# Kernel optimization log

Measured on AMD Instinct MI355X. Metric: run time of the kernel, lower is better.

Reference implementation:

```python
import jax, jax.numpy as jnp
import numpy as np

B, S, D = 4, 4096, 1024
DK, DV = 64, 64

def setup_inputs() -> dict:
    key = jax.random.key(0)
    ks = jax.random.split(key, 4)
    scale = 1.0 / np.sqrt(D)
    x = jax.random.normal(ks[0], (B, S, D), dtype=jnp.float32)
    Wq = jax.random.normal(ks[1], (DK, D), dtype=jnp.float32) * scale
    Wk = jax.random.normal(ks[2], (DK, D), dtype=jnp.float32) * scale
    Wv = jax.random.normal(ks[3], (DV, D), dtype=jnp.float32) * scale
    bq = jnp.zeros((DK,), jnp.float32)
    bk = jnp.zeros((DK,), jnp.float32)
    bv = jnp.zeros((DV,), jnp.float32)
    return {"x": x, "Wq": Wq, "bq": bq, "Wk": Wk, "bk": bk, "Wv": Wv, "bv": bv}

def reference(x, Wq, bq, Wk, bk, Wv, bv):
    # Linear projections (torch nn.Linear: y = x @ W.T + b)
    Q = jnp.einsum('bsd,kd->bsk', x, Wq) + bq      # [B,S,DK]
    K = jnp.einsum('bsd,kd->bsk', x, Wk) + bk      # [B,S,DK]
    V = jnp.einsum('bsd,vd->bsv', x, Wv) + bv      # [B,S,DV]
    scale = 1.0 / jnp.sqrt(jnp.float32(DK))
    scores = jnp.einsum('bqk,bsk->bqs', Q, K) * scale  # [B,S,S]
    attn = jax.nn.softmax(scores, axis=-1)
    return jnp.einsum('bqs,bsv->bqv', attn, V)     # [B,S,DV]
```

## Files before the change

### kernel.cpp

```cpp
#include <hip/hip_runtime.h>

typedef unsigned int uint;
typedef unsigned short ushort;

#define SQ 4096
#define DMODEL 1024
#define DH 64
#define NQ 16384
#define L2E 1.4426950408889634f
#define QSCALE (0.125f * 1.4426950408889634f)

typedef __attribute__((ext_vector_type(4))) float f32x4;
typedef __attribute__((ext_vector_type(8))) short bf16x8;

#if __has_builtin(__builtin_amdgcn_exp2f)
#define EXP2(x) __builtin_amdgcn_exp2f(x)
#else
#define EXP2(x) exp2f(x)
#endif


__device__ __forceinline__ void ld_lds16(const ushort* g, ushort* l) {
    __builtin_amdgcn_global_load_lds(
        (const __attribute__((address_space(1))) void*)g,
        (__attribute__((address_space(3))) void*)l, 16, 0, 0);
}

__device__ __forceinline__ void split2(float x, ushort& h, ushort& l) {
    uint u = __float_as_uint(x);
    float lof = x - __uint_as_float(u & 0xffff0000u);
    h = (ushort)(u >> 16);
    l = (ushort)(__float_as_uint(lof) >> 16);
}

__device__ __forceinline__ ushort bf16rne(float a) {
    uint ua = __float_as_uint(a);
    return (ushort)((ua + 0x7fffu + ((ua >> 16) & 1u)) >> 16);
}

__device__ __forceinline__ uint bfpack_rne(float a, float b) {
    uint ua = __float_as_uint(a);
    ua = (ua + 0x7fffu + ((ua >> 16) & 1u)) >> 16;
    uint ub = __float_as_uint(b);
    ub = (ub + 0x7fffu + ((ub >> 16) & 1u)) & 0xffff0000u;
    return ua | ub;
}

__global__ __launch_bounds__(256) void wsplit_kernel(
    const float* __restrict__ Wq, const float* __restrict__ Wk,
    const float* __restrict__ Wv, ushort* __restrict__ Wch)
{
    int r = blockIdx.x;
    int k = threadIdx.x * 4;
    const float* src = (r < 64)  ? (Wq + r * DMODEL)
                     : (r < 128) ? (Wk + (r - 64) * DMODEL)
                     :             (Wv + (r - 128) * DMODEL);
    float4 v = *(const float4*)&src[k];
    ushort h[4] = {bf16rne(v.x), bf16rne(v.y), bf16rne(v.z), bf16rne(v.w)};
    int ch = k >> 6, kl = k & 63;
    int g = kl >> 3;
    int idx = ch * 12288 + r * 64 + ((g ^ (r & 7)) << 3) + (kl & 7);
    *(ushort4*)&Wch[idx] = make_ushort4(h[0], h[1], h[2], h[3]);
}

__global__ __launch_bounds__(256, 1) void proj_kernel(
    const float* __restrict__ x, const ushort* __restrict__ Wch,
    const float* __restrict__ bq, const float* __restrict__ bk,
    const float* __restrict__ bv,
    ushort* __restrict__ Qr, ushort* __restrict__ Kr,
    ushort* __restrict__ Vh, ushort* __restrict__ Vl)
{
    extern __shared__ ushort sm[];

    const int tid  = threadIdx.x;
    const int w    = tid >> 6;
    const int l    = tid & 63;
    const int ln   = l & 15;
    const int quad = l >> 4;
    const int r0   = blockIdx.x << 6;
    const int xr   = tid >> 4;
    const int xc4  = tid & 15;

    f32x4 o_[4][3];
    #pragma unroll
    for (int mt = 0; mt < 4; ++mt)
        #pragma unroll
        for (int nt = 0; nt < 3; ++nt) o_[mt][nt] = (f32x4)0.f;

    float4 xv[4];
    #pragma unroll
    for (int i = 0; i < 4; ++i)
        xv[i] = *(const float4*)&x[(r0 + i * 16 + xr) * DMODEL + xc4 * 4];
    {
        const ushort* gh = Wch + w * 3072 + l * 8;
        ushort* dh = sm + 16384 + w * 3072;
        #pragma unroll
        for (int i = 0; i < 6; ++i) ld_lds16(gh + i * 512, dh + i * 512);
    }
    #pragma unroll
    for (int i = 0; i < 4; ++i) {
        int r = i * 16 + xr;
        ushort h0, h1, h2, h3, l0, l1, l2, l3;
        split2(xv[i].x, h0, l0); split2(xv[i].y, h1, l1);
        split2(xv[i].z, h2, l2); split2(xv[i].w, h3, l3);
        int idx = r * 64 + (((xc4 >> 1) ^ (r & 7)) << 3) + (xc4 & 1) * 4;
        *(ushort4*)&sm[idx]        = make_ushort4(h0, h1, h2, h3);
        *(ushort4*)&sm[4096 + idx] = make_ushort4(l0, l1, l2, l3);
    }

    for (int ch = 0; ch < 16; ++ch) {
        const int cur = ch & 1, nxt = cur ^ 1;
        __syncthreads();
        if (ch + 1 < 16) {
            const ushort* gh = Wch + (ch + 1) * 12288 + w * 3072 + l * 8;
            ushort* dh = sm + 16384 + nxt * 12288 + w * 3072;
            #pragma unroll
            for (int i = 0; i < 6; ++i) ld_lds16(gh + i * 512, dh + i * 512);
            #pragma unroll
            for (int i = 0; i < 4; ++i)
                xv[i] = *(const float4*)&x[(r0 + i * 16 + xr) * DMODEL +
                                           (ch + 1) * 64 + xc4 * 4];
        }
        const ushort* Xh = sm + cur * 8192;
        const ushort* Xl = Xh + 4096;
        const ushort* Wh = sm + 16384 + cur * 12288;
        #pragma unroll
        for (int kc = 0; kc < 2; ++kc) {
            int gsw = ((kc * 4 + quad) ^ (ln & 7)) << 3;
            bf16x8 xh[4], xl[4], wh[3];
            #pragma unroll
            for (int mt = 0; mt < 4; ++mt) {
                int off = (mt * 16 + ln) * 64 + gsw;
                xh[mt] = *(bf16x8*)&Xh[off];
                xl[mt] = *(bf16x8*)&Xl[off];
            }
            #pragma unroll
            for (int nt = 0; nt < 3; ++nt)
                wh[nt] = *(bf16x8*)&Wh[(w * 48 + nt * 16 + ln) * 64 + gsw];
            #pragma unroll
            for (int mt = 0; mt < 4; ++mt)
                #pragma unroll
                for (int nt = 0; nt < 3; ++nt) {
                    o_[mt][nt] = __builtin_amdgcn_mfma_f32_16x16x32_bf16(
                        xh[mt], wh[nt], o_[mt][nt], 0, 0, 0);
                    o_[mt][nt] = __builtin_amdgcn_mfma_f32_16x16x32_bf16(
                        xl[mt], wh[nt], o_[mt][nt], 0, 0, 0);
                }
        }
        if (ch + 1 < 16) {
            #pragma unroll
            for (int i = 0; i < 4; ++i) {
                int r = i * 16 + xr;
                ushort h0, h1, h2, h3, l0, l1, l2, l3;
                split2(xv[i].x, h0, l0); split2(xv[i].y, h1, l1);
                split2(xv[i].z, h2, l2); split2(xv[i].w, h3, l3);
                int idx = nxt * 8192 + r * 64 +
                          (((xc4 >> 1) ^ (r & 7)) << 3) + (xc4 & 1) * 4;
                *(ushort4*)&sm[idx]        = make_ushort4(h0, h1, h2, h3);
                *(ushort4*)&sm[4096 + idx] = make_ushort4(l0, l1, l2, l3);
            }
        }
    }

    __syncthreads();
    uint* Oqk = (uint*)sm;
    uint* Ov  = (uint*)sm + 8192;
    #pragma unroll
    for (int nt = 0; nt < 3; ++nt) {
        int col = 16 * (3 * w + nt) + ln;
        float bias, scl;
        if (col < 64)       { bias = bq[col];       scl = QSCALE; }
        else if (col < 128) { bias = bk[col - 64];  scl = 1.f; }
        else                { bias = bv[col - 128]; scl = 1.f; }
        #pragma unroll
        for (int mt = 0; mt < 4; ++mt)
            #pragma unroll
            for (int j = 0; j < 4; ++j) {
                int m = mt * 16 + quad * 4 + j;
                float val = (o_[mt][nt][j] + bias) * scl;
                if (col < 128) {
                    Oqk[m * 128 + col] = (uint)bf16rne(val);
                } else {
                    int v = col - 128;
                    uint u = __float_as_uint(val);
                    float lof = val - __uint_as_float(u & 0xffff0000u);
                    Ov[v * 64 + (m ^ ((v & 7) << 2))] =
                        (__float_as_uint(lof) & 0xffff0000u) | (u >> 16);
                }
            }
    }
    __syncthreads();
    const int tile_qk = r0 >> 6;
    #pragma unroll
    for (int i = 0; i < 8; ++i) {
        int id = i * 256 + tid;
        int m = id >> 5, g = id & 31;
        uint4 e = *(uint4*)&Oqk[m * 128 + g * 4];
        uint h0 = (e.x & 0xffffu) | (e.y << 16);
        uint h1 = (e.z & 0xffffu) | (e.w << 16);
        int gg = g & 15;
        int idx = tile_qk * 4096 + m * 64 +
                  (((gg >> 1) ^ (m & 7)) << 3) + (gg & 1) * 4;
        uint2 hh; hh.x = h0; hh.y = h1;
        if (g < 16) *(uint2*)&Qr[idx] = hh;
        else        *(uint2*)&Kr[idx] = hh;
    }
    const int b  = r0 >> 12;
    const int vt = b * 64 + ((r0 & (SQ - 1)) >> 6);
    #pragma unroll
    for (int i = 0; i < 4; ++i) {
        int id = i * 256 + tid;
        int v = id >> 4, gm = id & 15;
        uint4 e = *(uint4*)&Ov[v * 64 + 4 * (gm ^ (v & 7))];
        uint h0 = (e.x & 0xffffu) | (e.y << 16);
        uint h1 = (e.z & 0xffffu) | (e.w << 16);
        uint l0 = (e.x >> 16) | (e.y & 0xffff0000u);
        uint l1 = (e.z >> 16) | (e.w & 0xffff0000u);
        int idx = vt * 4096 + v * 64 + (((gm >> 1) ^ (v & 7)) << 3) + (gm & 1) * 4;
        uint2 hh; hh.x = h0; hh.y = h1;
        uint2 llv; llv.x = l0; llv.y = l1;
        *(uint2*)&Vh[idx] = hh; *(uint2*)&Vl[idx] = llv;
    }
}

__global__ __launch_bounds__(256, 2) void attn_kernel(
    const ushort* __restrict__ Qr, const ushort* __restrict__ Kr,
    const ushort* __restrict__ Vh, const ushort* __restrict__ Vl,
    float* __restrict__ opart, float* __restrict__ lpart,
    float* __restrict__ out, int ks)
{
    __shared__ ushort As[32768];

    const int tid  = threadIdx.x;
    const int w    = tid >> 6;
    const int l    = tid & 63;
    const int ln   = l & 15;
    const int quad = l >> 4;

    const int bid   = blockIdx.x;
    const int qb    = bid / ks;
    const int c     = bid - qb * ks;
    const int q0    = qb << 7;
    const int b     = q0 >> 12;
    const int chunk = SQ / ks;
    const int tile0 = (b * SQ + c * chunk) >> 6;
    const int vt0   = b * 64 + ((c * chunk) >> 6);
    const int nIter = chunk >> 6;

    {
        const ushort* gq = Qr + (q0 >> 6) * 4096 + w * 2048 + l * 8;
        #pragma unroll
        for (int i = 0; i < 4; ++i)
            ld_lds16(gq + i * 512, As + w * 2048 + i * 512);
    }
    __syncthreads();
    bf16x8 qf[2][2];
    #pragma unroll
    for (int nt = 0; nt < 2; ++nt)
        #pragma unroll
        for (int kc = 0; kc < 2; ++kc) {
            int row = w * 32 + nt * 16 + ln;
            qf[nt][kc] = *(bf16x8*)&As[row * 64 +
                                       (((kc * 4 + quad) ^ (ln & 7)) << 3)];
        }
    __syncthreads();

    {
        int kt = tile0 * 4096 + w * 1024 + l * 8;
        int vt = vt0 * 4096 + w * 1024 + l * 8;
        ld_lds16(Kr + kt,       As + w * 1024);
        ld_lds16(Kr + kt + 512, As + w * 1024 + 512);
        ld_lds16(Vh + vt,       As + 4096 + w * 1024);
        ld_lds16(Vh + vt + 512, As + 4096 + w * 1024 + 512);
        ld_lds16(Vl + vt,       As + 8192 + w * 1024);
        ld_lds16(Vl + vt + 512, As + 8192 + w * 1024 + 512);
    }

    float l_[2] = {0.f, 0.f};
    f32x4 o_[4][2];
    #pragma unroll
    for (int mt = 0; mt < 4; ++mt)
        #pragma unroll
        for (int nt = 0; nt < 2; ++nt) o_[mt][nt] = (f32x4)0.f;

    for (int it = 0; it < nIter; ++it) {
        const int cur = it & 1, nxt = cur ^ 1;
        __syncthreads();
        if (it + 1 < nIter) {
            int kt = (tile0 + it + 1) * 4096 + w * 1024 + l * 8;
            int vt = (vt0 + it + 1) * 4096 + w * 1024 + l * 8;
            ushort* bb = As + nxt * 12288;
            ld_lds16(Kr + kt,       bb + w * 1024);
            ld_lds16(Kr + kt + 512, bb + w * 1024 + 512);
            ld_lds16(Vh + vt,       bb + 4096 + w * 1024);
            ld_lds16(Vh + vt + 512, bb + 4096 + w * 1024 + 512);
            ld_lds16(Vl + vt,       bb + 8192 + w * 1024);
            ld_lds16(Vl + vt + 512, bb + 8192 + w * 1024 + 512);
        }
        const ushort* Ks  = As + cur * 12288;
        const ushort* Vhs = Ks + 4096;
        const ushort* Vls = Ks + 8192;
        ushort* Pw = As + 24576 + w * 2048;

        f32x4 s_[4][2];
        #pragma unroll
        for (int mt = 0; mt < 4; ++mt)
            #pragma unroll
            for (int nt = 0; nt < 2; ++nt) s_[mt][nt] = (f32x4)0.f;
        #pragma unroll
        for (int kc = 0; kc < 2; ++kc) {
            int gsw = ((kc * 4 + quad) ^ (ln & 7)) << 3;
            bf16x8 kah[4];
            #pragma unroll
            for (int mt = 0; mt < 4; ++mt)
                kah[mt] = *(bf16x8*)&Ks[(mt * 16 + ln) * 64 + gsw];
            #pragma unroll
            for (int mt = 0; mt < 4; ++mt)
                #pragma unroll
                for (int nt = 0; nt < 2; ++nt)
                    s_[mt][nt] = __builtin_amdgcn_mfma_f32_16x16x32_bf16(
                        kah[mt], qf[nt][kc], s_[mt][nt], 0, 0, 0);
        }

        #pragma unroll
        for (int nt = 0; nt < 2; ++nt) {
            #pragma unroll
            for (int mt = 0; mt < 4; ++mt)
                #pragma unroll
                for (int j = 0; j < 4; ++j) {
                    float p = EXP2(s_[mt][nt][j]);
                    s_[mt][nt][j] = p;
                    l_[nt] += p;
                }
            int q = ln + 16 * nt;
            int sw = ln & 7;
            #pragma unroll
            for (int mt = 0; mt < 4; ++mt) {
                uint e0 = bfpack_rne(s_[mt][nt][0], s_[mt][nt][1]);
                uint e1 = bfpack_rne(s_[mt][nt][2], s_[mt][nt][3]);
                int g = 2 * mt + (quad >> 1);
                int idx = q * 64 + ((g ^ sw) << 3) + (quad & 1) * 4;
                uint2 e; e.x = e0; e.y = e1;
                *(uint2*)&Pw[idx] = e;
            }
        }

        #pragma unroll
        for (int kc = 0; kc < 2; ++kc) {
            int gsw = ((kc * 4 + quad) ^ (ln & 7)) << 3;
            bf16x8 vah[4], vav[4], pb[2];
            #pragma unroll
            for (int mt = 0; mt < 4; ++mt) {
                int off = (mt * 16 + ln) * 64 + gsw;
                vah[mt] = *(bf16x8*)&Vhs[off];
                vav[mt] = *(bf16x8*)&Vls[off];
            }
            #pragma unroll
            for (int nt = 0; nt < 2; ++nt)
                pb[nt] = *(bf16x8*)&Pw[(ln + 16 * nt) * 64 + gsw];
            #pragma unroll
            for (int mt = 0; mt < 4; ++mt)
                #pragma unroll
                for (int nt = 0; nt < 2; ++nt) {
                    o_[mt][nt] = __builtin_amdgcn_mfma_f32_16x16x32_bf16(
                        vah[mt], pb[nt], o_[mt][nt], 0, 0, 0);
                    o_[mt][nt] = __builtin_amdgcn_mfma_f32_16x16x32_bf16(
                        vav[mt], pb[nt], o_[mt][nt], 0, 0, 0);
                }
        }
    }

    #pragma unroll
    for (int nt = 0; nt < 2; ++nt) {
        l_[nt] += __shfl_xor(l_[nt], 16);
        l_[nt] += __shfl_xor(l_[nt], 32);
    }
    __syncthreads();
    float* tr = (float*)(As + w * 4096);
    if (ks == 1) {
        #pragma unroll
        for (int nt = 0; nt < 2; ++nt) {
            float inv = 1.f / l_[nt];
            #pragma unroll
            for (int mt = 0; mt < 4; ++mt) o_[mt][nt] *= inv;
        }
    }
    #pragma unroll
    for (int p = 0; p < 2; ++p) {
        #pragma unroll
        for (int mt = 0; mt < 4; ++mt)
            #pragma unroll
            for (int j = 0; j < 4; ++j)
                tr[(ln * 16 + ((mt * 4 + quad) ^ ln)) * 4 + j] = o_[mt][p][j];
        #pragma unroll
        for (int i2 = 0; i2 < 4; ++i2) {
            int qt = i2 * 4 + quad;
            f32x4 vv = *(f32x4*)&tr[(qt * 16 + (ln ^ qt)) * 4];
            int qg = q0 + w * 32 + p * 16 + qt;
            if (ks == 1) *(f32x4*)&out[qg * DH + ln * 4] = vv;
            else *(f32x4*)&opart[((size_t)c * NQ + qg) * DH + ln * 4] = vv;
        }
    }
    if (ks > 1 && quad == 0) {
        #pragma unroll
        for (int nt = 0; nt < 2; ++nt) {
            int qg = q0 + w * 32 + 16 * nt + ln;
            lpart[c * NQ + qg] = l_[nt];
        }
    }
}

__global__ __launch_bounds__(256) void attn_combine(
    const float* __restrict__ opart, const float* __restrict__ lpart,
    float* __restrict__ out, int ks)
{
    int id = blockIdx.x * 256 + threadIdx.x;
    int q = id >> 4, c4 = id & 15;
    float den = 0.f;
    f32x4 num = (f32x4)0.f;
    for (int c = 0; c < ks; ++c) {
        den += lpart[c * NQ + q];
        num += *(const f32x4*)&opart[((size_t)c * NQ + q) * DH + c4 * 4];
    }
    float inv = 1.f / den;
    *(f32x4*)&out[q * DH + c4 * 4] = num * inv;
}

extern "C" void kernel_launch(void* const* d_in, const int* in_sizes, int n_in,
                              void* d_out, int out_size, void* d_ws, size_t ws_size,
                              hipStream_t stream) {
    const float* x  = (const float*)d_in[0];
    const float* Wq = (const float*)d_in[1];
    const float* bq = (const float*)d_in[2];
    const float* Wk = (const float*)d_in[3];
    const float* bk = (const float*)d_in[4];
    const float* Wv = (const float*)d_in[5];
    const float* bv = (const float*)d_in[6];
    float* out = (float*)d_out;

    const size_t n16 = (size_t)NQ * DH;
    char* p = (char*)d_ws;
    ushort* Qr = (ushort*)p;           p += n16 * 2;
    ushort* Kr = (ushort*)p;           p += n16 * 2;
    ushort* Vh = (ushort*)p;           p += n16 * 2;
    ushort* Vl = (ushort*)p;           p += n16 * 2;
    ushort* Wch = (ushort*)p;          p += 192 * 1024 * 2;

    size_t base = (size_t)(p - (char*)d_ws);
    int ks = 4;
    while (ks > 1 &&
           base + (size_t)ks * n16 * 4 + (size_t)ks * NQ * 4 > ws_size)
        ks >>= 1;

    float* opart = (float*)p;          p += (size_t)ks * n16 * 4;
    float* lpart = (float*)p;

    hipFuncSetAttribute((const void*)proj_kernel,
                        hipFuncAttributeMaxDynamicSharedMemorySize, 81920);

    wsplit_kernel<<<192, 256, 0, stream>>>(Wq, Wk, Wv, Wch);
    proj_kernel<<<NQ / 64, 256, 81920, stream>>>(x, Wch, bq, bk, bv,
                                                 Qr, Kr, Vh, Vl);
    attn_kernel<<<(NQ / 128) * ks, 256, 0, stream>>>(
        Qr, Kr, Vh, Vl, opart, lpart, out, ks);
    if (ks > 1)
        attn_combine<<<(NQ * 16) / 256, 256, 0, stream>>>(opart, lpart, out, ks);
}
```

Measured before the change: 171.6 us.

## Drop V hi/lo split, halve projection tile, raise occupancy and split-K

V is now stored as a single bf16 array instead of hi/lo bf16 pairs, which halves the V loads and the PV MFMAs in the attention kernel and frees LDS so three blocks can fit per CU. The projection kernel moves from 64 to 32 rows per block with static LDS and two blocks per CU. P and x are packed to bf16 by truncation through a perm instruction instead of round-to-nearest. The key split grows from 4 to 8, and exp2 goes through the ocml call. The precision of V and P drops, which risks accuracy, and the larger split adds more partial-sum traffic for the combine pass.

```diff
diff --git a/kernel.cpp b/kernel.cpp
--- a/kernel.cpp
+++ b/kernel.cpp
@@ -7,17 +7,10 @@
 #define DMODEL 1024
 #define DH 64
 #define NQ 16384
-#define L2E 1.4426950408889634f
 #define QSCALE (0.125f * 1.4426950408889634f)
 
 typedef __attribute__((ext_vector_type(4))) float f32x4;
 typedef __attribute__((ext_vector_type(8))) short bf16x8;
-
-#if __has_builtin(__builtin_amdgcn_exp2f)
-#define EXP2(x) __builtin_amdgcn_exp2f(x)
-#else
-#define EXP2(x) exp2f(x)
-#endif
 
 
 __device__ __forceinline__ void ld_lds16(const ushort* g, ushort* l) {
@@ -26,11 +19,13 @@
         (__attribute__((address_space(3))) void*)l, 16, 0, 0);
 }
 
-__device__ __forceinline__ void split2(float x, ushort& h, ushort& l) {
-    uint u = __float_as_uint(x);
-    float lof = x - __uint_as_float(u & 0xffff0000u);
-    h = (ushort)(u >> 16);
-    l = (ushort)(__float_as_uint(lof) >> 16);
+__device__ __forceinline__ uint pack2trunc(float a, float b) {
+#if __has_builtin(__builtin_amdgcn_perm)
+    return __builtin_amdgcn_perm(__float_as_uint(b), __float_as_uint(a),
+                                 0x07060302u);
+#else
+    return (__float_as_uint(a) >> 16) | (__float_as_uint(b) & 0xffff0000u);
+#endif
 }
 
 __device__ __forceinline__ ushort bf16rne(float a) {
@@ -38,13 +33,12 @@
     return (ushort)((ua + 0x7fffu + ((ua >> 16) & 1u)) >> 16);
 }
 
-__device__ __forceinline__ uint bfpack_rne(float a, float b) {
-    uint ua = __float_as_uint(a);
-    ua = (ua + 0x7fffu + ((ua >> 16) & 1u)) >> 16;
-    uint ub = __float_as_uint(b);
-    ub = (ub + 0x7fffu + ((ub >> 16) & 1u)) & 0xffff0000u;
-    return ua | ub;
-}
+#if defined(__HIP_DEVICE_COMPILE__)
+#define EXP2(x) __ocml_exp2_f32(x)
+extern "C" __device__ float __ocml_exp2_f32(float);
+#else
+#define EXP2(x) exp2f(x)
+#endif
 
 __global__ __launch_bounds__(256) void wsplit_kernel(
     const float* __restrict__ Wq, const float* __restrict__ Wk,
@@ -63,73 +57,74 @@
     *(ushort4*)&Wch[idx] = make_ushort4(h[0], h[1], h[2], h[3]);
 }
 
-__global__ __launch_bounds__(256, 1) void proj_kernel(
+__global__ __launch_bounds__(256, 2) void proj_kernel(
     const float* __restrict__ x, const ushort* __restrict__ Wch,
     const float* __restrict__ bq, const float* __restrict__ bk,
     const float* __restrict__ bv,
-    ushort* __restrict__ Qr, ushort* __restrict__ Kr,
-    ushort* __restrict__ Vh, ushort* __restrict__ Vl)
+    ushort* __restrict__ Qr, ushort* __restrict__ Kr, ushort* __restrict__ Vr)
 {
-    extern __shared__ ushort sm[];
+    __shared__ ushort sm[32768];
 
     const int tid  = threadIdx.x;
     const int w    = tid >> 6;
     const int l    = tid & 63;
     const int ln   = l & 15;
     const int quad = l >> 4;
-    const int r0   = blockIdx.x << 6;
-    const int xr   = tid >> 4;
-    const int xc4  = tid & 15;
-
-    f32x4 o_[4][3];
-    #pragma unroll
-    for (int mt = 0; mt < 4; ++mt)
+    const int r0   = blockIdx.x << 5;
+    const int xr   = tid >> 3;
+    const int xs   = tid & 7;
+    const int xidx = xr * 64 + ((xs ^ (xr & 7)) << 3);
+
+    f32x4 o_[2][3];
+    #pragma unroll
+    for (int mt = 0; mt < 2; ++mt)
         #pragma unroll
         for (int nt = 0; nt < 3; ++nt) o_[mt][nt] = (f32x4)0.f;
 
-    float4 xv[4];
-    #pragma unroll
-    for (int i = 0; i < 4; ++i)
-        xv[i] = *(const float4*)&x[(r0 + i * 16 + xr) * DMODEL + xc4 * 4];
+    float4 xa, xb;
+    xa = *(const float4*)&x[(r0 + xr) * DMODEL + xs * 8];
+    xb = *(const float4*)&x[(r0 + xr) * DMODEL + xs * 8 + 4];
     {
         const ushort* gh = Wch + w * 3072 + l * 8;
-        ushort* dh = sm + 16384 + w * 3072;
+        ushort* dh = sm + 8192 + w * 3072;
         #pragma unroll
         for (int i = 0; i < 6; ++i) ld_lds16(gh + i * 512, dh + i * 512);
     }
-    #pragma unroll
-    for (int i = 0; i < 4; ++i) {
-        int r = i * 16 + xr;
-        ushort h0, h1, h2, h3, l0, l1, l2, l3;
-        split2(xv[i].x, h0, l0); split2(xv[i].y, h1, l1);
-        split2(xv[i].z, h2, l2); split2(xv[i].w, h3, l3);
-        int idx = r * 64 + (((xc4 >> 1) ^ (r & 7)) << 3) + (xc4 & 1) * 4;
-        *(ushort4*)&sm[idx]        = make_ushort4(h0, h1, h2, h3);
-        *(ushort4*)&sm[4096 + idx] = make_ushort4(l0, l1, l2, l3);
+    {
+        float f[8] = {xa.x, xa.y, xa.z, xa.w, xb.x, xb.y, xb.z, xb.w};
+        uint hh[4], ll[4];
+        #pragma unroll
+        for (int n = 0; n < 4; ++n) {
+            float a = f[2 * n], b = f[2 * n + 1];
+            float la = a - __uint_as_float(__float_as_uint(a) & 0xffff0000u);
+            float lb = b - __uint_as_float(__float_as_uint(b) & 0xffff0000u);
+            hh[n] = pack2trunc(a, b);
+            ll[n] = pack2trunc(la, lb);
+        }
+        *(uint4*)&sm[xidx]        = make_uint4(hh[0], hh[1], hh[2], hh[3]);
+        *(uint4*)&sm[2048 + xidx] = make_uint4(ll[0], ll[1], ll[2], ll[3]);
     }
 
     for (int ch = 0; ch < 16; ++ch) {
         const int cur = ch & 1, nxt = cur ^ 1;
         __syncthreads();
         if (ch + 1 < 16) {
+            xa = *(const float4*)&x[(r0 + xr) * DMODEL + (ch + 1) * 64 + xs * 8];
+            xb = *(const float4*)&x[(r0 + xr) * DMODEL + (ch + 1) * 64 + xs * 8 + 4];
             const ushort* gh = Wch + (ch + 1) * 12288 + w * 3072 + l * 8;
-            ushort* dh = sm + 16384 + nxt * 12288 + w * 3072;
+            ushort* dh = sm + 8192 + nxt * 12288 + w * 3072;
             #pragma unroll
             for (int i = 0; i < 6; ++i) ld_lds16(gh + i * 512, dh + i * 512);
-            #pragma unroll
-            for (int i = 0; i < 4; ++i)
-                xv[i] = *(const float4*)&x[(r0 + i * 16 + xr) * DMODEL +
-                                           (ch + 1) * 64 + xc4 * 4];
-        }
-        const ushort* Xh = sm + cur * 8192;
-        const ushort* Xl = Xh + 4096;
-        const ushort* Wh = sm + 16384 + cur * 12288;
+        }
+        const ushort* Xh = sm + cur * 4096;
+        const ushort* Xl = Xh + 2048;
+        const ushort* Wh = sm + 8192 + cur * 12288;
         #pragma unroll
         for (int kc = 0; kc < 2; ++kc) {
             int gsw = ((kc * 4 + quad) ^ (ln & 7)) << 3;
-            bf16x8 xh[4], xl[4], wh[3];
-            #pragma unroll
-            for (int mt = 0; mt < 4; ++mt) {
+            bf16x8 xh[2], xl[2], wh[3];
+            #pragma unroll
+            for (int mt = 0; mt < 2; ++mt) {
                 int off = (mt * 16 + ln) * 64 + gsw;
                 xh[mt] = *(bf16x8*)&Xh[off];
                 xl[mt] = *(bf16x8*)&Xl[off];
@@ -138,7 +133,7 @@
             for (int nt = 0; nt < 3; ++nt)
                 wh[nt] = *(bf16x8*)&Wh[(w * 48 + nt * 16 + ln) * 64 + gsw];
             #pragma unroll
-            for (int mt = 0; mt < 4; ++mt)
+            for (int mt = 0; mt < 2; ++mt)
                 #pragma unroll
                 for (int nt = 0; nt < 3; ++nt) {
                     o_[mt][nt] = __builtin_amdgcn_mfma_f32_16x16x32_bf16(
@@ -148,23 +143,26 @@
                 }
         }
         if (ch + 1 < 16) {
-            #pragma unroll
-            for (int i = 0; i < 4; ++i) {
-                int r = i * 16 + xr;
-                ushort h0, h1, h2, h3, l0, l1, l2, l3;
-                split2(xv[i].x, h0, l0); split2(xv[i].y, h1, l1);
-                split2(xv[i].z, h2, l2); split2(xv[i].w, h3, l3);
-                int idx = nxt * 8192 + r * 64 +
-                          (((xc4 >> 1) ^ (r & 7)) << 3) + (xc4 & 1) * 4;
-                *(ushort4*)&sm[idx]        = make_ushort4(h0, h1, h2, h3);
-                *(ushort4*)&sm[4096 + idx] = make_ushort4(l0, l1, l2, l3);
+            float f[8] = {xa.x, xa.y, xa.z, xa.w, xb.x, xb.y, xb.z, xb.w};
+            uint hh[4], ll[4];
+            #pragma unroll
+            for (int n = 0; n < 4; ++n) {
+                float a = f[2 * n], b = f[2 * n + 1];
+                float la = a - __uint_as_float(__float_as_uint(a) & 0xffff0000u);
+                float lb = b - __uint_as_float(__float_as_uint(b) & 0xffff0000u);
+                hh[n] = pack2trunc(a, b);
+                ll[n] = pack2trunc(la, lb);
             }
+            *(uint4*)&sm[nxt * 4096 + xidx] =
+                make_uint4(hh[0], hh[1], hh[2], hh[3]);
+            *(uint4*)&sm[nxt * 4096 + 2048 + xidx] =
+                make_uint4(ll[0], ll[1], ll[2], ll[3]);
         }
     }
 
     __syncthreads();
     uint* Oqk = (uint*)sm;
-    uint* Ov  = (uint*)sm + 8192;
+    uint* Ov  = (uint*)sm + 4096;
     #pragma unroll
     for (int nt = 0; nt < 3; ++nt) {
         int col = 16 * (3 * w + nt) + ln;
@@ -173,63 +171,58 @@
         else if (col < 128) { bias = bk[col - 64];  scl = 1.f; }
         else                { bias = bv[col - 128]; scl = 1.f; }
         #pragma unroll
-        for (int mt = 0; mt < 4; ++mt)
+        for (int mt = 0; mt < 2; ++mt)
             #pragma unroll
             for (int j = 0; j < 4; ++j) {
                 int m = mt * 16 + quad * 4 + j;
                 float val = (o_[mt][nt][j] + bias) * scl;
-                if (col < 128) {
-                    Oqk[m * 128 + col] = (uint)bf16rne(val);
-                } else {
+                if (col < 128) Oqk[m * 128 + col] = (uint)bf16rne(val);
+                else {
                     int v = col - 128;
-                    uint u = __float_as_uint(val);
-                    float lof = val - __uint_as_float(u & 0xffff0000u);
-                    Ov[v * 64 + (m ^ ((v & 7) << 2))] =
-                        (__float_as_uint(lof) & 0xffff0000u) | (u >> 16);
+                    Ov[v * 32 + (m ^ ((v & 7) << 2))] = (uint)bf16rne(val);
                 }
             }
     }
     __syncthreads();
     const int tile_qk = r0 >> 6;
-    #pragma unroll
-    for (int i = 0; i < 8; ++i) {
+    const int half    = r0 & 32;
+    #pragma unroll
+    for (int i = 0; i < 4; ++i) {
         int id = i * 256 + tid;
         int m = id >> 5, g = id & 31;
         uint4 e = *(uint4*)&Oqk[m * 128 + g * 4];
-        uint h0 = (e.x & 0xffffu) | (e.y << 16);
-        uint h1 = (e.z & 0xffffu) | (e.w << 16);
+        uint2 hh;
+        hh.x = e.x | (e.y << 16);
+        hh.y = e.z | (e.w << 16);
         int gg = g & 15;
-        int idx = tile_qk * 4096 + m * 64 +
+        int row = half + m;
+        int idx = tile_qk * 4096 + row * 64 +
                   (((gg >> 1) ^ (m & 7)) << 3) + (gg & 1) * 4;
-        uint2 hh; hh.x = h0; hh.y = h1;
         if (g < 16) *(uint2*)&Qr[idx] = hh;
         else        *(uint2*)&Kr[idx] = hh;
     }
-    const int b  = r0 >> 12;
-    const int vt = b * 64 + ((r0 & (SQ - 1)) >> 6);
-    #pragma unroll
-    for (int i = 0; i < 4; ++i) {
+    const int vt = (r0 >> 12) * 64 + ((r0 & (SQ - 1)) >> 6);
+    #pragma unroll
+    for (int i = 0; i < 2; ++i) {
         int id = i * 256 + tid;
-        int v = id >> 4, gm = id & 15;
-        uint4 e = *(uint4*)&Ov[v * 64 + 4 * (gm ^ (v & 7))];
-        uint h0 = (e.x & 0xffffu) | (e.y << 16);
-        uint h1 = (e.z & 0xffffu) | (e.w << 16);
-        uint l0 = (e.x >> 16) | (e.y & 0xffff0000u);
-        uint l1 = (e.z >> 16) | (e.w & 0xffff0000u);
-        int idx = vt * 4096 + v * 64 + (((gm >> 1) ^ (v & 7)) << 3) + (gm & 1) * 4;
-        uint2 hh; hh.x = h0; hh.y = h1;
-        uint2 llv; llv.x = l0; llv.y = l1;
-        *(uint2*)&Vh[idx] = hh; *(uint2*)&Vl[idx] = llv;
-    }
-}
-
-__global__ __launch_bounds__(256, 2) void attn_kernel(
+        int v = id >> 3, gm = id & 7;
+        uint4 e = *(uint4*)&Ov[v * 32 + ((gm ^ (v & 7)) << 2)];
+        uint2 hh;
+        hh.x = e.x | (e.y << 16);
+        hh.y = e.z | (e.w << 16);
+        int tg = (half >> 3) + (gm >> 1);
+        int idx = vt * 4096 + v * 64 + ((tg ^ (v & 7)) << 3) + (gm & 1) * 4;
+        *(uint2*)&Vr[idx] = hh;
+    }
+}
+
+__global__ __launch_bounds__(256, 3) void attn_kernel(
     const ushort* __restrict__ Qr, const ushort* __restrict__ Kr,
-    const ushort* __restrict__ Vh, const ushort* __restrict__ Vl,
+    const ushort* __restrict__ Vr,
     float* __restrict__ opart, float* __restrict__ lpart,
     float* __restrict__ out, int ks)
 {
-    __shared__ ushort As[32768];
+    __shared__ ushort As[24576];
 
     const int tid  = threadIdx.x;
     const int w    = tid >> 6;
@@ -270,10 +263,8 @@
         int vt = vt0 * 4096 + w * 1024 + l * 8;
         ld_lds16(Kr + kt,       As + w * 1024);
         ld_lds16(Kr + kt + 512, As + w * 1024 + 512);
-        ld_lds16(Vh + vt,       As + 4096 + w * 1024);
-        ld_lds16(Vh + vt + 512, As + 4096 + w * 1024 + 512);
-        ld_lds16(Vl + vt,       As + 8192 + w * 1024);
-        ld_lds16(Vl + vt + 512, As + 8192 + w * 1024 + 512);
+        ld_lds16(Vr + vt,       As + 4096 + w * 1024);
+        ld_lds16(Vr + vt + 512, As + 4096 + w * 1024 + 512);
     }
 
     float l_[2] = {0.f, 0.f};
@@ -289,18 +280,15 @@
         if (it + 1 < nIter) {
             int kt = (tile0 + it + 1) * 4096 + w * 1024 + l * 8;
             int vt = (vt0 + it + 1) * 4096 + w * 1024 + l * 8;
-            ushort* bb = As + nxt * 12288;
+            ushort* bb = As + nxt * 8192;
             ld_lds16(Kr + kt,       bb + w * 1024);
             ld_lds16(Kr + kt + 512, bb + w * 1024 + 512);
-            ld_lds16(Vh + vt,       bb + 4096 + w * 1024);
-            ld_lds16(Vh + vt + 512, bb + 4096 + w * 1024 + 512);
-            ld_lds16(Vl + vt,       bb + 8192 + w * 1024);
-            ld_lds16(Vl + vt + 512, bb + 8192 + w * 1024 + 512);
-        }
-        const ushort* Ks  = As + cur * 12288;
-        const ushort* Vhs = Ks + 4096;
-        const ushort* Vls = Ks + 8192;
-        ushort* Pw = As + 24576 + w * 2048;
+            ld_lds16(Vr + vt,       bb + 4096 + w * 1024);
+            ld_lds16(Vr + vt + 512, bb + 4096 + w * 1024 + 512);
+        }
+        const ushort* Ks = As + cur * 8192;
+        const ushort* Vs = Ks + 4096;
+        ushort* Pw = As + 16384 + w * 2048;
 
         f32x4 s_[4][2];
         #pragma unroll
@@ -336,37 +324,30 @@
             int sw = ln & 7;
             #pragma unroll
             for (int mt = 0; mt < 4; ++mt) {
-                uint e0 = bfpack_rne(s_[mt][nt][0], s_[mt][nt][1]);
-                uint e1 = bfpack_rne(s_[mt][nt][2], s_[mt][nt][3]);
+                uint2 e;
+                e.x = pack2trunc(s_[mt][nt][0], s_[mt][nt][1]);
+                e.y = pack2trunc(s_[mt][nt][2], s_[mt][nt][3]);
                 int g = 2 * mt + (quad >> 1);
-                int idx = q * 64 + ((g ^ sw) << 3) + (quad & 1) * 4;
-                uint2 e; e.x = e0; e.y = e1;
-                *(uint2*)&Pw[idx] = e;
+                *(uint2*)&Pw[q * 64 + ((g ^ sw) << 3) + (quad & 1) * 4] = e;
             }
         }
 
         #pragma unroll
         for (int kc = 0; kc < 2; ++kc) {
             int gsw = ((kc * 4 + quad) ^ (ln & 7)) << 3;
-            bf16x8 vah[4], vav[4], pb[2];
-            #pragma unroll
-            for (int mt = 0; mt < 4; ++mt) {
-                int off = (mt * 16 + ln) * 64 + gsw;
-                vah[mt] = *(bf16x8*)&Vhs[off];
-                vav[mt] = *(bf16x8*)&Vls[off];
-            }
+            bf16x8 vah[4], pb[2];
+            #pragma unroll
+            for (int mt = 0; mt < 4; ++mt)
+                vah[mt] = *(bf16x8*)&Vs[(mt * 16 + ln) * 64 + gsw];
             #pragma unroll
             for (int nt = 0; nt < 2; ++nt)
                 pb[nt] = *(bf16x8*)&Pw[(ln + 16 * nt) * 64 + gsw];
             #pragma unroll
             for (int mt = 0; mt < 4; ++mt)
                 #pragma unroll
-                for (int nt = 0; nt < 2; ++nt) {
+                for (int nt = 0; nt < 2; ++nt)
                     o_[mt][nt] = __builtin_amdgcn_mfma_f32_16x16x32_bf16(
                         vah[mt], pb[nt], o_[mt][nt], 0, 0, 0);
-                    o_[mt][nt] = __builtin_amdgcn_mfma_f32_16x16x32_bf16(
-                        vav[mt], pb[nt], o_[mt][nt], 0, 0, 0);
-                }
         }
     }
 
@@ -442,12 +423,11 @@
     char* p = (char*)d_ws;
     ushort* Qr = (ushort*)p;           p += n16 * 2;
     ushort* Kr = (ushort*)p;           p += n16 * 2;
-    ushort* Vh = (ushort*)p;           p += n16 * 2;
-    ushort* Vl = (ushort*)p;           p += n16 * 2;
+    ushort* Vr = (ushort*)p;           p += n16 * 2;
     ushort* Wch = (ushort*)p;          p += 192 * 1024 * 2;
 
     size_t base = (size_t)(p - (char*)d_ws);
-    int ks = 4;
+    int ks = 8;
     while (ks > 1 &&
            base + (size_t)ks * n16 * 4 + (size_t)ks * NQ * 4 > ws_size)
         ks >>= 1;
@@ -455,14 +435,10 @@
     float* opart = (float*)p;          p += (size_t)ks * n16 * 4;
     float* lpart = (float*)p;
 
-    hipFuncSetAttribute((const void*)proj_kernel,
-                        hipFuncAttributeMaxDynamicSharedMemorySize, 81920);
-
     wsplit_kernel<<<192, 256, 0, stream>>>(Wq, Wk, Wv, Wch);
-    proj_kernel<<<NQ / 64, 256, 81920, stream>>>(x, Wch, bq, bk, bv,
-                                                 Qr, Kr, Vh, Vl);
+    proj_kernel<<<NQ / 32, 256, 0, stream>>>(x, Wch, bq, bk, bv, Qr, Kr, Vr);
     attn_kernel<<<(NQ / 128) * ks, 256, 0, stream>>>(
-        Qr, Kr, Vh, Vl, opart, lpart, out, ks);
+        Qr, Kr, Vr, opart, lpart, out, ks);
     if (ks > 1)
         attn_combine<<<(NQ * 16) / 256, 256, 0, stream>>>(opart, lpart, out, ks);
 }
```

Result: faster. 159.5 us (-7.1%).
